# Kernel optimization log

Measured on AMD Instinct MI355X. Metric: run time of the kernel, lower is better.

The kernel has to match this reference:

```python
import jax, jax.numpy as jnp
import numpy as np

B, L, D, KSIZE = 8, 2048, 768, 8


def setup_inputs() -> dict:
    key = jax.random.key(0)
    k1, k2, k3, k4, k5 = jax.random.split(key, 5)
    s = 1.0 / np.sqrt(D)  # torch default GRU init scale
    x = jax.random.normal(k1, (B, L, D), dtype=jnp.float32)
    w_ih = jax.random.uniform(k2, (D, 3 * D), jnp.float32, -s, s)
    w_hh = jax.random.uniform(k3, (D, 3 * D), jnp.float32, -s, s)
    b_ih = jax.random.uniform(k4, (3 * D,), jnp.float32, -s, s)
    b_hh = jax.random.uniform(k5, (3 * D,), jnp.float32, -s, s)
    return {"x": x, "w_ih": w_ih, "w_hh": w_hh, "b_ih": b_ih, "b_hh": b_hh, "ksize": KSIZE}


def reference(x, w_ih, w_hh, b_ih, b_hh, ksize):
    """LocalRNN forward: sliding window of size ksize (zero left-pad), GRU over
    each window, return last hidden state per position -> [B, L, D].
    Instead of materializing the redundant [B*L, ksize, D] windowed tensor,
    we run the ksize-step recurrence over all positions in parallel: the j-th
    GRU step for window ending at t consumes xpad[:, t + j, :].
    """
    Bb, Ll, Dd = x.shape
    xpad = jnp.concatenate([jnp.zeros((Bb, ksize - 1, Dd), x.dtype), x], axis=1)
    # precompute input-side gate activations once: [B, L+k-1, 3D]
    gx_all = xpad @ w_ih + b_ih

    def step(h, j):
        gx = jax.lax.dynamic_slice_in_dim(gx_all, j, Ll, axis=1)  # [B, L, 3D]
        gh = h @ w_hh + b_hh                                       # [B, L, 3D]
        xr, xz, xn = jnp.split(gx, 3, axis=-1)
        hr, hz, hn = jnp.split(gh, 3, axis=-1)
        r = jax.nn.sigmoid(xr + hr)
        z = jax.nn.sigmoid(xz + hz)
        n = jnp.tanh(xn + r * hn)
        h_new = (1.0 - z) * n + z * h
        return h_new, None

    h0 = jnp.zeros((Bb, Ll, Dd), x.dtype)
    h, _ = jax.lax.scan(step, h0, jnp.arange(ksize))
    return h
```

## Files before the change

### kernel.cpp

```cpp
#include <hip/hip_runtime.h>
#include <stdint.h>
#include <stddef.h>

using short8 = __attribute__((ext_vector_type(8))) short;
using f32x4  = __attribute__((ext_vector_type(4))) float;

#define BB 8
#define LL 2048
#define DD 768
#define KS 8
#define ND 2304
#define NT 12
#define NBN_GX 18

__device__ __forceinline__ float bf2f(unsigned short u) {
  union { uint32_t i; float f; } v; v.i = ((uint32_t)u) << 16; return v.f;
}
__device__ __forceinline__ unsigned short f2bf(float f) {
  union { float f; uint32_t i; } v; v.f = f;
  return (unsigned short)((v.i + 0x7FFFu + ((v.i >> 16) & 1u)) >> 16);
}
__device__ __forceinline__ float sigm(float x) { return 1.0f / (1.0f + __expf(-x)); }
__device__ __forceinline__ float tanh_fast(float x) {
  return 2.0f / (1.0f + __expf(-2.0f * x)) - 1.0f;
}
__device__ __forceinline__ void gload_lds16(const void* g, void* lds) {
  __builtin_amdgcn_global_load_lds(
      (const __attribute__((address_space(1))) void*)g,
      (__attribute__((address_space(3))) void*)lds, 16, 0, 0);
}

__device__ __forceinline__ void swz_blocks(int bid, int nbm, int nbn,
                                           int* mb, int* nb) {
  int gsz = 8 * nbn;
  int g = bid / gsz;
  int rem = bid - g * gsz;
  int gg = nbm - g * 8; if (gg > 8) gg = 8;
  *nb = rem / gg;
  *mb = g * 8 + (rem - *nb * gg);
}

__global__ void detect_k(const uint32_t* __restrict__ x, int* __restrict__ flag) {
  int t = threadIdx.x;
  uint32_t w = x[t * 16];
  int e = (int)((w >> 7) & 0xFF);
  int isbf = (e >= 112 && e <= 136) ? 1 : 0;
  unsigned long long m = __ballot(isbf);
  if (t == 0) *flag = (__popcll(m) >= 32) ? 1 : 0;
}

__global__ void transpose_k(const void* __restrict__ in,
                            unsigned short* __restrict__ out, int R, int C,
                            const int* __restrict__ flagp) {
  const bool bf = (*flagp != 0);
  __shared__ unsigned short t[32][33];
  int c0 = blockIdx.x * 32, r0 = blockIdx.y * 32;
  int tx = threadIdx.x, ty = threadIdx.y;
#pragma unroll
  for (int i = ty; i < 32; i += 8) {
    size_t idx = (size_t)(r0 + i) * C + c0 + tx;
    t[i][tx] = bf ? ((const unsigned short*)in)[idx]
                  : f2bf(((const float*)in)[idx]);
  }
  __syncthreads();
#pragma unroll
  for (int i = ty; i < 32; i += 8)
    out[(size_t)(c0 + i) * R + r0 + tx] = t[tx][i];
}

__global__ void conv_bias(const void* __restrict__ in,
                          unsigned short* __restrict__ out, int n,
                          const int* __restrict__ flagp) {
  const bool bf = (*flagp != 0);
  int i = blockIdx.x * 256 + threadIdx.x;
  if (i >= n) return;
  out[i] = bf ? ((const unsigned short*)in)[i] : f2bf(((const float*)in)[i]);
}

__global__ void conv_x(const void* __restrict__ xv,
                       unsigned short* __restrict__ xpadc,
                       int Uc, int t0, int total8,
                       const int* __restrict__ flagp) {
  const bool bf = (*flagp != 0);
  int idx = blockIdx.x * 256 + threadIdx.x;
  if (idx >= total8) return;
  size_t e = (size_t)idx * 8;
  int d = (int)(e % DD);
  size_t ru = e / DD;
  int u = (int)(ru % Uc);
  int b = (int)(ru / Uc);
  int p = t0 + u;
  short8 v = {0, 0, 0, 0, 0, 0, 0, 0};
  if (p >= KS - 1) {
    size_t base = ((size_t)b * LL + (p - (KS - 1))) * DD + d;
    if (bf) {
      v = *(const short8*)((const unsigned short*)xv + base);
    } else {
      const float* fp = (const float*)xv + base;
      float4 a = *(const float4*)fp, b4 = *(const float4*)(fp + 4);
      v[0] = (short)f2bf(a.x); v[1] = (short)f2bf(a.y);
      v[2] = (short)f2bf(a.z); v[3] = (short)f2bf(a.w);
      v[4] = (short)f2bf(b4.x); v[5] = (short)f2bf(b4.y);
      v[6] = (short)f2bf(b4.z); v[7] = (short)f2bf(b4.w);
    }
  }
  *(short8*)&xpadc[e] = v;
}

__global__ __launch_bounds__(256, 3) void gemm_gx(
    const unsigned short* __restrict__ A, const unsigned short* __restrict__ WT,
    const unsigned short* __restrict__ bias, unsigned short* __restrict__ Cout,
    int Mrows, int nbm) {
  __shared__ __align__(16) unsigned short Al[128 * 64];
  __shared__ __align__(16) unsigned short Bl[128 * 64];
  const int tid = threadIdx.x, lane = tid & 63, wv = tid >> 6;
  const int wm = wv >> 1, wn = wv & 1;
  int mb, nb; swz_blocks(blockIdx.x, nbm, NBN_GX, &mb, &nb);
  const int m0 = mb * 128, n0 = nb * 128;
  const int h16 = lane >> 4, l16 = lane & 15;

  const unsigned short* asrc[4];
  const unsigned short* bsrc[4];
#pragma unroll
  for (int it = 0; it < 4; ++it) {
    int c = it * 256 + tid;
    int row = c >> 3;
    int slotg = (c & 7) ^ (row & 7);
    int grow = m0 + row; if (grow >= Mrows) grow = Mrows - 1;
    asrc[it] = A + (size_t)grow * DD + slotg * 8;
    bsrc[it] = WT + (size_t)(n0 + row) * DD + slotg * 8;
  }
  char* aldst = (char*)Al + (wv * 1024);
  char* bldst = (char*)Bl + (wv * 1024);

  f32x4 acc[4][4] = {};

  for (int kt = 0; kt < NT; ++kt) {
    const int ko = kt * 64;
#pragma unroll
    for (int it = 0; it < 4; ++it)
      gload_lds16(asrc[it] + ko, aldst + it * 4096);
#pragma unroll
    for (int it = 0; it < 4; ++it)
      gload_lds16(bsrc[it] + ko, bldst + it * 4096);
    __syncthreads();
#pragma unroll
    for (int s = 0; s < 2; ++s) {
      short8 af[4], bfr[4];
#pragma unroll
      for (int i = 0; i < 4; ++i) {
        int row = wm * 64 + i * 16 + l16;
        af[i] = *(const short8*)&Al[row * 64 + (((s * 4 + h16) ^ (row & 7)) * 8)];
      }
#pragma unroll
      for (int jn = 0; jn < 4; ++jn) {
        int row = wn * 64 + jn * 16 + l16;
        bfr[jn] = *(const short8*)&Bl[row * 64 + (((s * 4 + h16) ^ (row & 7)) * 8)];
      }
#pragma unroll
      for (int i = 0; i < 4; ++i)
#pragma unroll
        for (int jn = 0; jn < 4; ++jn)
          acc[i][jn] = __builtin_amdgcn_mfma_f32_16x16x32_bf16(af[i], bfr[jn], acc[i][jn], 0, 0, 0);
    }
    if (kt + 1 < NT) __syncthreads();
  }

#pragma unroll
  for (int jn = 0; jn < 4; ++jn) {
    int n = n0 + wn * 64 + jn * 16 + l16;
    float bv = bf2f(bias[n]);
#pragma unroll
    for (int i = 0; i < 4; ++i) {
      int mb2 = m0 + wm * 64 + i * 16 + 4 * h16;
#pragma unroll
      for (int r = 0; r < 4; ++r) {
        int m = mb2 + r;
        if (m < Mrows) Cout[(size_t)m * ND + n] = f2bf(acc[i][jn][r] + bv);
      }
    }
  }
}

__global__ void gru_step0(const unsigned short* __restrict__ gx, int Uc,
                          const unsigned short* __restrict__ bhh,
                          unsigned short* __restrict__ hout, int lgTc) {
  int idx = blockIdx.x * 256 + threadIdx.x;
  int d = idx % DD;
  int row = idx / DD;
  int b = row >> lgTc, t = row & ((1 << lgTc) - 1);
  size_t gxrow = ((size_t)b * Uc + t) * ND;
  float xr = bf2f(gx[gxrow + d]);
  float xz = bf2f(gx[gxrow + DD + d]);
  float xn = bf2f(gx[gxrow + 2 * DD + d]);
  float br = bf2f(bhh[d]), bz = bf2f(bhh[DD + d]), bn = bf2f(bhh[2 * DD + d]);
  float r = sigm(xr + br);
  float z = sigm(xz + bz);
  float n = tanh_fast(xn + r * bn);
  hout[(size_t)row * DD + d] = f2bf((1.0f - z) * n);
}

__global__ __launch_bounds__(256, 3) void gemm_gru_step(
    const unsigned short* __restrict__ Hc, const unsigned short* __restrict__ WT,
    const unsigned short* __restrict__ bhh, const unsigned short* __restrict__ gx,
    int Uc, void* __restrict__ Hn, int hnBS, int hnOff, int j, int lgTc,
    const int* __restrict__ flagp, int isFinal) {
  __shared__ __align__(16) unsigned short Al[128 * 64];
  __shared__ __align__(16) unsigned short Bl[192 * 64];
  const bool bfm = (*flagp != 0);
  const int tid = threadIdx.x, lane = tid & 63, wv = tid >> 6;
  const int wm = wv >> 1, wd = wv & 1;
  const int m0 = blockIdx.x * 128, d0 = blockIdx.y * 64;
  const int h16 = lane >> 4, l16 = lane & 15;
  const int tmask = (1 << lgTc) - 1;

  const unsigned short* asrc[4];
#pragma unroll
  for (int it = 0; it < 4; ++it) {
    int c = it * 256 + tid;
    int row = c >> 3;
    int slotg = (c & 7) ^ (row & 7);
    asrc[it] = Hc + (size_t)(m0 + row) * DD + slotg * 8;
  }
  const unsigned short* bsrc[6];
#pragma unroll
  for (int it = 0; it < 6; ++it) {
    int c = it * 256 + tid;
    int row = c >> 3;
    int g = row >> 6;
    int wrow = g * DD + d0 + (row & 63);
    int slotg = (c & 7) ^ (row & 7);
    bsrc[it] = WT + (size_t)wrow * DD + slotg * 8;
  }
  char* aldst = (char*)Al + (wv * 1024);
  char* bldst = (char*)Bl + (wv * 1024);

  f32x4 acc[4][2][3] = {};

  for (int kt = 0; kt < NT; ++kt) {
    const int ko = kt * 64;
#pragma unroll
    for (int it = 0; it < 4; ++it)
      gload_lds16(asrc[it] + ko, aldst + it * 4096);
#pragma unroll
    for (int it = 0; it < 6; ++it)
      gload_lds16(bsrc[it] + ko, bldst + it * 4096);
    __syncthreads();
#pragma unroll
    for (int s = 0; s < 2; ++s) {
      short8 af[4];
#pragma unroll
      for (int i = 0; i < 4; ++i) {
        int row = wm * 64 + i * 16 + l16;
        af[i] = *(const short8*)&Al[row * 64 + (((s * 4 + h16) ^ (row & 7)) * 8)];
      }
      short8 bfr[2][3];
#pragma unroll
      for (int jd = 0; jd < 2; ++jd)
#pragma unroll
        for (int g = 0; g < 3; ++g) {
          int row = g * 64 + wd * 32 + jd * 16 + l16;
          bfr[jd][g] = *(const short8*)&Bl[row * 64 + (((s * 4 + h16) ^ (row & 7)) * 8)];
        }
#pragma unroll
      for (int i = 0; i < 4; ++i)
#pragma unroll
        for (int jd = 0; jd < 2; ++jd)
#pragma unroll
          for (int g = 0; g < 3; ++g)
            acc[i][jd][g] = __builtin_amdgcn_mfma_f32_16x16x32_bf16(af[i], bfr[jd][g], acc[i][jd][g], 0, 0, 0);
    }
    if (kt + 1 < NT) __syncthreads();
  }

#pragma unroll
  for (int jd = 0; jd < 2; ++jd) {
    int d = d0 + wd * 32 + jd * 16 + l16;
    float br = bf2f(bhh[d]), bz = bf2f(bhh[DD + d]), bn = bf2f(bhh[2 * DD + d]);
#pragma unroll
    for (int i = 0; i < 4; ++i) {
      int mbase = m0 + wm * 64 + i * 16 + 4 * h16;
#pragma unroll
      for (int r2 = 0; r2 < 4; ++r2) {
        int m = mbase + r2;
        int b = m >> lgTc, t = m & tmask;
        size_t gxrow = ((size_t)b * Uc + t + j) * ND;
        float xr = bf2f(gx[gxrow + d]);
        float xz = bf2f(gx[gxrow + DD + d]);
        float xn = bf2f(gx[gxrow + 2 * DD + d]);
        float gr = acc[i][jd][0][r2] + br;
        float gz = acc[i][jd][1][r2] + bz;
        float gn = acc[i][jd][2][r2] + bn;
        float rr = sigm(xr + gr);
        float zz = sigm(xz + gz);
        float nn = tanh_fast(xn + rr * gn);
        float ho = bf2f(Hc[(size_t)m * DD + d]);
        float val = (1.0f - zz) * nn + zz * ho;
        size_t hnrow = (size_t)b * hnBS + hnOff + t;
        if (isFinal && !bfm) ((float*)Hn)[hnrow * DD + d] = val;
        else ((unsigned short*)Hn)[hnrow * DD + d] = f2bf(val);
      }
    }
  }
}

extern "C" void kernel_launch(void* const* d_in, const int* in_sizes, int n_in,
                              void* d_out, int out_size, void* d_ws, size_t ws_size,
                              hipStream_t stream) {
  const void* x    = d_in[0];
  const void* w_ih = d_in[1];
  const void* w_hh = d_in[2];
  const void* b_ih = d_in[3];
  const void* b_hh = d_in[4];

  const size_t wTbytes = (size_t)ND * DD * 2;
  const size_t hdr = 2 * wTbytes + 2 * 4608 + 4096;

  int Tc = 64;
  for (int tc = 2048; tc >= 64; tc >>= 1) {
    size_t hBsz  = (size_t)BB * tc * DD * 2;
    size_t xpsz  = (size_t)BB * (tc + KS - 1) * DD * 2;
    size_t uni   = hBsz > xpsz ? hBsz : xpsz;
    size_t need = hdr +
                  (size_t)BB * (tc + KS - 1) * ND * 2 +
                  (size_t)BB * tc * DD * 2 +
                  uni;
    if (need <= ws_size) { Tc = tc; break; }
  }
  int lgTc = 0; while ((1 << lgTc) < Tc) ++lgTc;
  const int Uc = Tc + KS - 1;
  const int Mc = BB * Tc;
  const int Mg = BB * Uc;

  char* ws = (char*)d_ws;
  unsigned short* wihT = (unsigned short*)ws; ws += wTbytes;
  unsigned short* whhT = (unsigned short*)ws; ws += wTbytes;
  unsigned short* bihB = (unsigned short*)ws; ws += 4608;
  unsigned short* bhhB = (unsigned short*)ws; ws += 4608;
  int* flag            = (int*)ws;            ws += 4096;
  unsigned short* gxc  = (unsigned short*)ws; ws += (size_t)Mg * ND * 2;
  unsigned short* hA   = (unsigned short*)ws; ws += (size_t)Mc * DD * 2;
  unsigned short* hB   = (unsigned short*)ws;
  unsigned short* xpadc = hB;

  detect_k<<<1, 64, 0, stream>>>((const uint32_t*)x, flag);
  transpose_k<<<dim3(ND / 32, DD / 32), dim3(32, 8), 0, stream>>>(w_ih, wihT, DD, ND, flag);
  transpose_k<<<dim3(ND / 32, DD / 32), dim3(32, 8), 0, stream>>>(w_hh, whhT, DD, ND, flag);
  conv_bias<<<(ND + 255) / 256, 256, 0, stream>>>(b_ih, bihB, ND, flag);
  conv_bias<<<(ND + 255) / 256, 256, 0, stream>>>(b_hh, bhhB, ND, flag);

  const int nbmGx = (Mg + 127) / 128;

  for (int t0 = 0; t0 < LL; t0 += Tc) {
    int total8 = Mg * (DD / 8);
    conv_x<<<(total8 + 255) / 256, 256, 0, stream>>>(x, xpadc, Uc, t0, total8, flag);

    gemm_gx<<<nbmGx * NBN_GX, 256, 0, stream>>>(
        xpadc, wihT, bihB, gxc, Mg, nbmGx);

    gru_step0<<<(Mc * DD) / 256, 256, 0, stream>>>(gxc, Uc, bhhB, hA, lgTc);

    unsigned short* cur = hA;
    for (int j = 1; j <= 7; ++j) {
      int isFinal = (j == 7);
      void* dst = isFinal ? d_out : (void*)((cur == hA) ? hB : hA);
      int hnBS = isFinal ? LL : Tc;
      int hnOff = isFinal ? t0 : 0;
      gemm_gru_step<<<dim3(Mc / 128, DD / 64), 256, 0, stream>>>(
          cur, whhT, bhhB, gxc, Uc, dst, hnBS, hnOff, j, lgTc, flag, isFinal);
      if (!isFinal) cur = (cur == hA) ? hB : hA;
    }
  }
}
```

Baseline: 741.9 us.

## Double-buffer LDS tiles with prefetch two k-steps ahead in both GEMMs

Both the input-gate GEMM and the fused GRU-step GEMM now keep two LDS buffers and issue the global-to-LDS loads for tile kt+2 while tile kt is being computed. They wait with explicit vmcnt counts instead of a full sync after each load. This is meant to hide global memory latency behind the MFMA work. In exchange LDS per block doubles and the launch bound drops from 3 to 2 blocks per CU, which lowers occupancy.

New measurement: 808.0 us. 8.9% more time.

```diff
diff --git a/kernel.cpp b/kernel.cpp
--- a/kernel.cpp
+++ b/kernel.cpp
@@ -107,12 +107,12 @@
   *(short8*)&xpadc[e] = v;
 }
 
-__global__ __launch_bounds__(256, 3) void gemm_gx(
+__global__ __launch_bounds__(256, 2) void gemm_gx(
     const unsigned short* __restrict__ A, const unsigned short* __restrict__ WT,
     const unsigned short* __restrict__ bias, unsigned short* __restrict__ Cout,
     int Mrows, int nbm) {
-  __shared__ __align__(16) unsigned short Al[128 * 64];
-  __shared__ __align__(16) unsigned short Bl[128 * 64];
+  __shared__ __align__(16) unsigned short Al[2][128 * 64];
+  __shared__ __align__(16) unsigned short Bl[2][128 * 64];
   const int tid = threadIdx.x, lane = tid & 63, wv = tid >> 6;
   const int wm = wv >> 1, wn = wv & 1;
   int mb, nb; swz_blocks(blockIdx.x, nbm, NBN_GX, &mb, &nb);
@@ -130,32 +130,42 @@
     asrc[it] = A + (size_t)grow * DD + slotg * 8;
     bsrc[it] = WT + (size_t)(n0 + row) * DD + slotg * 8;
   }
-  char* aldst = (char*)Al + (wv * 1024);
-  char* bldst = (char*)Bl + (wv * 1024);
+
+#define GX_ISSUE(KT, BUF)                                                     \
+  {                                                                           \
+    const int ko_ = (KT) * 64;                                                \
+    _Pragma("unroll")                                                         \
+    for (int it = 0; it < 4; ++it)                                            \
+      gload_lds16(asrc[it] + ko_, (char*)Al[BUF] + wv * 1024 + it * 4096);    \
+    _Pragma("unroll")                                                         \
+    for (int it = 0; it < 4; ++it)                                            \
+      gload_lds16(bsrc[it] + ko_, (char*)Bl[BUF] + wv * 1024 + it * 4096);    \
+  }
 
   f32x4 acc[4][4] = {};
 
+  GX_ISSUE(0, 0);
+  GX_ISSUE(1, 1);
+
   for (int kt = 0; kt < NT; ++kt) {
-    const int ko = kt * 64;
-#pragma unroll
-    for (int it = 0; it < 4; ++it)
-      gload_lds16(asrc[it] + ko, aldst + it * 4096);
-#pragma unroll
-    for (int it = 0; it < 4; ++it)
-      gload_lds16(bsrc[it] + ko, bldst + it * 4096);
-    __syncthreads();
+    if (kt < NT - 1) asm volatile("s_waitcnt vmcnt(8)" ::: "memory");
+    else             asm volatile("s_waitcnt vmcnt(0)" ::: "memory");
+    __builtin_amdgcn_s_barrier();
+    __builtin_amdgcn_sched_barrier(0);
+    const unsigned short* Ab = Al[kt & 1];
+    const unsigned short* Bb = Bl[kt & 1];
 #pragma unroll
     for (int s = 0; s < 2; ++s) {
       short8 af[4], bfr[4];
 #pragma unroll
       for (int i = 0; i < 4; ++i) {
         int row = wm * 64 + i * 16 + l16;
-        af[i] = *(const short8*)&Al[row * 64 + (((s * 4 + h16) ^ (row & 7)) * 8)];
+        af[i] = *(const short8*)&Ab[row * 64 + (((s * 4 + h16) ^ (row & 7)) * 8)];
       }
 #pragma unroll
       for (int jn = 0; jn < 4; ++jn) {
         int row = wn * 64 + jn * 16 + l16;
-        bfr[jn] = *(const short8*)&Bl[row * 64 + (((s * 4 + h16) ^ (row & 7)) * 8)];
+        bfr[jn] = *(const short8*)&Bb[row * 64 + (((s * 4 + h16) ^ (row & 7)) * 8)];
       }
 #pragma unroll
       for (int i = 0; i < 4; ++i)
@@ -163,8 +173,13 @@
         for (int jn = 0; jn < 4; ++jn)
           acc[i][jn] = __builtin_amdgcn_mfma_f32_16x16x32_bf16(af[i], bfr[jn], acc[i][jn], 0, 0, 0);
     }
-    if (kt + 1 < NT) __syncthreads();
-  }
+    __builtin_amdgcn_sched_barrier(0);
+    if (kt + 2 < NT) {
+      __builtin_amdgcn_s_barrier();
+      GX_ISSUE(kt + 2, kt & 1);
+    }
+  }
+#undef GX_ISSUE
 
 #pragma unroll
   for (int jn = 0; jn < 4; ++jn) {
@@ -200,13 +215,13 @@
   hout[(size_t)row * DD + d] = f2bf((1.0f - z) * n);
 }
 
-__global__ __launch_bounds__(256, 3) void gemm_gru_step(
+__global__ __launch_bounds__(256, 2) void gemm_gru_step(
     const unsigned short* __restrict__ Hc, const unsigned short* __restrict__ WT,
     const unsigned short* __restrict__ bhh, const unsigned short* __restrict__ gx,
     int Uc, void* __restrict__ Hn, int hnBS, int hnOff, int j, int lgTc,
     const int* __restrict__ flagp, int isFinal) {
-  __shared__ __align__(16) unsigned short Al[128 * 64];
-  __shared__ __align__(16) unsigned short Bl[192 * 64];
+  __shared__ __align__(16) unsigned short Al[2][128 * 64];
+  __shared__ __align__(16) unsigned short Bl[2][192 * 64];
   const bool bfm = (*flagp != 0);
   const int tid = threadIdx.x, lane = tid & 63, wv = tid >> 6;
   const int wm = wv >> 1, wd = wv & 1;
@@ -232,27 +247,37 @@
     int slotg = (c & 7) ^ (row & 7);
     bsrc[it] = WT + (size_t)wrow * DD + slotg * 8;
   }
-  char* aldst = (char*)Al + (wv * 1024);
-  char* bldst = (char*)Bl + (wv * 1024);
+
+#define GRU_ISSUE(KT, BUF)                                                    \
+  {                                                                           \
+    const int ko_ = (KT) * 64;                                                \
+    _Pragma("unroll")                                                         \
+    for (int it = 0; it < 4; ++it)                                            \
+      gload_lds16(asrc[it] + ko_, (char*)Al[BUF] + wv * 1024 + it * 4096);    \
+    _Pragma("unroll")                                                         \
+    for (int it = 0; it < 6; ++it)                                            \
+      gload_lds16(bsrc[it] + ko_, (char*)Bl[BUF] + wv * 1024 + it * 4096);    \
+  }
 
   f32x4 acc[4][2][3] = {};
 
+  GRU_ISSUE(0, 0);
+  GRU_ISSUE(1, 1);
+
   for (int kt = 0; kt < NT; ++kt) {
-    const int ko = kt * 64;
-#pragma unroll
-    for (int it = 0; it < 4; ++it)
-      gload_lds16(asrc[it] + ko, aldst + it * 4096);
-#pragma unroll
-    for (int it = 0; it < 6; ++it)
-      gload_lds16(bsrc[it] + ko, bldst + it * 4096);
-    __syncthreads();
+    if (kt < NT - 1) asm volatile("s_waitcnt vmcnt(10)" ::: "memory");
+    else             asm volatile("s_waitcnt vmcnt(0)" ::: "memory");
+    __builtin_amdgcn_s_barrier();
+    __builtin_amdgcn_sched_barrier(0);
+    const unsigned short* Ab = Al[kt & 1];
+    const unsigned short* Bb = Bl[kt & 1];
 #pragma unroll
     for (int s = 0; s < 2; ++s) {
       short8 af[4];
 #pragma unroll
       for (int i = 0; i < 4; ++i) {
         int row = wm * 64 + i * 16 + l16;
-        af[i] = *(const short8*)&Al[row * 64 + (((s * 4 + h16) ^ (row & 7)) * 8)];
+        af[i] = *(const short8*)&Ab[row * 64 + (((s * 4 + h16) ^ (row & 7)) * 8)];
       }
       short8 bfr[2][3];
 #pragma unroll
@@ -260,7 +285,7 @@
 #pragma unroll
         for (int g = 0; g < 3; ++g) {
           int row = g * 64 + wd * 32 + jd * 16 + l16;
-          bfr[jd][g] = *(const short8*)&Bl[row * 64 + (((s * 4 + h16) ^ (row & 7)) * 8)];
+          bfr[jd][g] = *(const short8*)&Bb[row * 64 + (((s * 4 + h16) ^ (row & 7)) * 8)];
         }
 #pragma unroll
       for (int i = 0; i < 4; ++i)
@@ -270,8 +295,13 @@
           for (int g = 0; g < 3; ++g)
             acc[i][jd][g] = __builtin_amdgcn_mfma_f32_16x16x32_bf16(af[i], bfr[jd][g], acc[i][jd][g], 0, 0, 0);
     }
-    if (kt + 1 < NT) __syncthreads();
-  }
+    __builtin_amdgcn_sched_barrier(0);
+    if (kt + 2 < NT) {
+      __builtin_amdgcn_s_barrier();
+      GRU_ISSUE(kt + 2, kt & 1);
+    }
+  }
+#undef GRU_ISSUE
 
 #pragma unroll
   for (int jd = 0; jd < 2; ++jd) {
```
